# Performance work log

Measured on AMD Instinct MI355X. Metric: run time of the kernel, lower is better.

Reference implementation:

```python
import jax, jax.numpy as jnp
import numpy as np

NA, NM, H, RBF = 50000, 16384, 128, 64
GX, GY, GZ, B = 8, 8, 8, 32  # NM = B * GX*GY*GZ
E_AA, E_AM, E_MA = 800000, 400000, 400000
EPS = 1e-5


def setup_inputs() -> dict:
    key = jax.random.key(0)
    k = jax.random.split(key, 24)
    r = lambda i, s: jax.random.normal(k[i], s, jnp.float32)
    u = lambda i, s: jax.random.uniform(k[i], s, jnp.float32)
    ri = lambda i, s, hi: jax.random.randint(k[i], s, 0, hi, jnp.int32)
    return {
        "a_x": r(0, (NA, H)),
        "m_x": r(1, (NM, H)),
        "a2a_edge_index": ri(2, (2, E_AA), NA),
        "a2m_src": ri(3, (E_AM,), NA), "a2m_dst": ri(4, (E_AM,), NM),
        "m2a_src": ri(5, (E_MA,), NM), "m2a_dst": ri(6, (E_MA,), NA),
        "a2a_edge_weights": u(7, (E_AA,)),
        "a2m_edge_weights": u(8, (E_AM,)),
        "m2a_edge_weights": u(9, (E_MA,)),
        "a2a_edge_attr": r(10, (E_AA, RBF)),
        "a2m_edge_attr": r(11, (E_AM, RBF)),
        "m2a_edge_attr": r(12, (E_MA, RBF)),
        # message-passing params (node proj + RBF edge filter) per branch
        "W_short": r(13, (H, H)) / np.sqrt(H), "We_short": r(14, (RBF, H)) / np.sqrt(RBF),
        "W_a2m": r(15, (H, H)) / np.sqrt(H),  "We_a2m": r(16, (RBF, H)) / np.sqrt(RBF),
        "W_m2a": r(17, (H, H)) / np.sqrt(H),  "We_m2a": r(18, (RBF, H)) / np.sqrt(RBF),
        # long-range Conv3d (kernel 3, SAME padding)
        "conv_k": r(19, (H, H, 3, 3, 3)) / np.sqrt(H * 27), "conv_b": jnp.zeros((H,), jnp.float32),
        # LayerNorm affine params
        "g_short": jnp.ones((H,), jnp.float32), "b_short": jnp.zeros((H,), jnp.float32),
        "g_long": jnp.ones((H,), jnp.float32),  "b_long": jnp.zeros((H,), jnp.float32),
        "g_a2m": jnp.ones((H,), jnp.float32),   "b_a2m": jnp.zeros((H,), jnp.float32),
        "g_m2a": jnp.ones((H,), jnp.float32),   "b_m2a": jnp.zeros((H,), jnp.float32),
    }


def _ln(x, g, b):
    mu = x.mean(-1, keepdims=True)
    var = ((x - mu) ** 2).mean(-1, keepdims=True)
    return (x - mu) * jax.lax.rsqrt(var + EPS) * g + b


def _mp(x, src, dst, ew, ea, W, We, dim_size):
    # continuous-filter message pass: msg_e = (W x_src) * (We rbf_e) * w_e ; scatter-sum
    msg = (x[src] @ W) * (ea @ We) * ew[:, None]  # [E, H]
    return jax.ops.segment_sum(msg, dst, num_segments=dim_size)


def reference(a_x, m_x, a2a_edge_index, a2m_src, a2m_dst, m2a_src, m2a_dst,
              a2a_edge_weights, a2m_edge_weights, m2a_edge_weights,
              a2a_edge_attr, a2m_edge_attr, m2a_edge_attr,
              W_short, We_short, W_a2m, We_a2m, W_m2a, We_m2a,
              conv_k, conv_b,
              g_short, b_short, g_long, b_long, g_a2m, b_a2m, g_m2a, b_m2a):
    delta_a, delta_m = a_x, m_x
    # short-range atom branch
    a = _ln(a_x, g_short, b_short)
    a = _mp(a, a2a_edge_index[0], a2a_edge_index[1], a2a_edge_weights,
            a2a_edge_attr, W_short, We_short, NA)
    # long-range mesh branch: LN -> grid Conv3d (NCDHW) -> flatten back
    m = _ln(m_x, g_long, b_long)
    grid = m.reshape(B, GX, GY, GZ, H).transpose(0, 4, 1, 2, 3)  # [B,H,gx,gy,gz]
    grid = jax.lax.conv_general_dilated(
        grid, conv_k, window_strides=(1, 1, 1), padding='SAME',
        dimension_numbers=('NCDHW', 'OIDHW', 'NCDHW')) + conv_b[None, :, None, None, None]
    m = grid.transpose(0, 2, 3, 4, 1).reshape(-1, H)
    # cross messages with post-LN
    a2m_msg = _ln(_mp(a, a2m_src, a2m_dst, a2m_edge_weights, a2m_edge_attr,
                      W_a2m, We_a2m, NM), g_a2m, b_a2m)
    m2a_msg = _ln(_mp(m, m2a_src, m2a_dst, m2a_edge_weights, m2a_edge_attr,
                      W_m2a, We_m2a, NA), g_m2a, b_m2a)
    return (a + m2a_msg + delta_a, m + a2m_msg + delta_m)
```

## Files before the change

### kernel.cpp

```cpp
#include <hip/hip_runtime.h>
#include <hip/hip_bf16.h>

#define H 128
#define RBF 64

typedef __attribute__((ext_vector_type(8))) short bf16x8;
typedef __attribute__((ext_vector_type(4))) float f32x4;

__device__ inline short f2bf(float f) {
  union { float f; unsigned u; } v; v.f = f;
  const unsigned r = (v.u + 0x7FFFu + ((v.u >> 16) & 1u)) >> 16;
  return (short)r;
}

__global__ __launch_bounds__(128) void ln_rows(const float* __restrict__ X,
                                               const float* __restrict__ g,
                                               const float* __restrict__ bb,
                                               float* __restrict__ Y, int N) {
  __shared__ float sh[4];
  const int row = blockIdx.x;
  const int j = threadIdx.x;
  float x = X[(size_t)row * H + j];
  float s = x, q = x * x;
#pragma unroll
  for (int m = 32; m; m >>= 1) {
    s += __shfl_xor(s, m, 64);
    q += __shfl_xor(q, m, 64);
  }
  if ((j & 63) == 0) { sh[(j >> 6) * 2] = s; sh[(j >> 6) * 2 + 1] = q; }
  __syncthreads();
  s = sh[0] + sh[2];
  q = sh[1] + sh[3];
  const float mu = s * 0.0078125f;
  const float var = q * 0.0078125f - mu * mu;
  const float rs = rsqrtf(var + 1e-5f);
  Y[(size_t)row * H + j] = (x - mu) * rs * g[j] + bb[j];
}

__global__ __launch_bounds__(256) void pack_kt(const float* __restrict__ K,
                                               short* __restrict__ Ktb) {
  const int id = blockIdx.x * 256 + threadIdx.x;
  if (id >= 27 * 4 * 8 * 64) return;
  const int l = id & 63;
  int r = id >> 6;
  const int cb = r & 7; r >>= 3;
  const int kb = r & 3;
  const int tap = r >> 2;
  const int o = cb * 16 + (l & 15);
  const int i0 = kb * 32 + (l >> 4) * 8;
  short* out = Ktb + (size_t)id * 8;
#pragma unroll
  for (int j = 0; j < 8; ++j)
    out[j] = f2bf(K[((size_t)o * H + i0 + j) * 27 + tap]);
}

__global__ __launch_bounds__(256) void pack_we3(
    const float* __restrict__ We0, const float* __restrict__ We1,
    const float* __restrict__ We2, short* __restrict__ Wb0,
    short* __restrict__ Wb1, short* __restrict__ Wb2) {
  const int id = blockIdx.x * 256 + threadIdx.x;
  if (id >= 3072) return;
  const int which = id >> 10;
  const int i = id & 1023;
  const float* We = which == 0 ? We0 : which == 1 ? We1 : We2;
  short* Web = which == 0 ? Wb0 : which == 1 ? Wb1 : Wb2;
  const int f = i >> 6, l = i & 63;
  const int h = f >> 3, c = f & 7;
  const int col = (c << 4) + (l & 15);
  const int k0 = h * 32 + (l >> 4) * 8;
  short* o = Web + (size_t)i * 8;
#pragma unroll
  for (int j = 0; j < 8; ++j) o[j] = f2bf(We[(k0 + j) * H + col]);
}

__global__ __launch_bounds__(256) void k_hist3(
    const int* __restrict__ d0, const int* __restrict__ d1,
    const int* __restrict__ d2, int E0, int E1, int E2,
    int* __restrict__ cnt, int off1, int off2) {
  int i = blockIdx.x * 256 + threadIdx.x;
  const int stride = gridDim.x * 256;
  const int ET = E0 + E1 + E2;
  for (; i < ET; i += stride) {
    int d, off;
    if (i < E0) { d = d0[i]; off = 0; }
    else if (i < E0 + E1) { d = d1[i - E0]; off = off1; }
    else { d = d2[i - E0 - E1]; off = off2; }
    atomicAdd(&cnt[off + d], 1);
  }
}

__global__ __launch_bounds__(256) void k_blocksum(const int* __restrict__ cnt,
                                                  int* __restrict__ bsum) {
  __shared__ int sh[256];
  const int t = threadIdx.x;
  sh[t] = cnt[blockIdx.x * 256 + t];
  __syncthreads();
#pragma unroll
  for (int o = 128; o; o >>= 1) {
    if (t < o) sh[t] += sh[t + o];
    __syncthreads();
  }
  if (!t) bsum[blockIdx.x] = sh[0];
}

__global__ __launch_bounds__(512) void k_scan512(const int* __restrict__ bsum,
                                                 int* __restrict__ bpre, int NB) {
  __shared__ int sh[512];
  const int t = threadIdx.x;
  const int v = (t < NB) ? bsum[t] : 0;
  sh[t] = v;
  __syncthreads();
  for (int o = 1; o < 512; o <<= 1) {
    const int u = (t >= o) ? sh[t - o] : 0;
    __syncthreads();
    sh[t] += u;
    __syncthreads();
  }
  if (t < NB) bpre[t] = sh[t] - v;
}

__global__ __launch_bounds__(256) void k_apply3(
    const int* __restrict__ cnt, const int* __restrict__ bpre,
    int* __restrict__ rp0, int* __restrict__ rp1, int* __restrict__ rp2,
    int* __restrict__ cursor, int N0, int N1, int N2, int S1, int S2) {
  __shared__ int sh[256];
  const int b = blockIdx.x;
  const int t = threadIdx.x;
  const int gi = b * 256 + t;
  const int v = cnt[gi];
  sh[t] = v;
  __syncthreads();
  for (int o = 1; o < 256; o <<= 1) {
    const int u = (t >= o) ? sh[t - o] : 0;
    __syncthreads();
    sh[t] += u;
    __syncthreads();
  }
  int sb, N;
  int* rp;
  if (b < S1) { sb = 0; N = N0; rp = rp0; }
  else if (b < S2) { sb = S1; N = N1; rp = rp1; }
  else { sb = S2; N = N2; rp = rp2; }
  const int excl = sh[t] - v + bpre[b] - bpre[sb];
  const int il = (b - sb) * 256 + t;
  if (il <= N) {
    rp[il] = excl;
    if (il < N) cursor[gi] = excl;
  }
}

__global__ __launch_bounds__(256) void k_perm2w(
    const int* __restrict__ dst, const int* __restrict__ src,
    const float* __restrict__ ew, const float* __restrict__ ea, int E,
    int* __restrict__ cursor, int2* __restrict__ sd,
    short* __restrict__ eapfp) {
  const int lane = threadIdx.x & 63;
  const int wid = blockIdx.x * 4 + (threadIdx.x >> 6);
  const int nw = gridDim.x * 4;
  if (blockIdx.x == 0 && threadIdx.x < 16)
    sd[E + threadIdx.x] = make_int2(0, -1);
  const int r = lane >> 2;
  const int c = lane & 3;
  for (int ebase = wid * 16; ebase < E; ebase += nw * 16) {
    const int ecnt = min(16, E - ebase);
    int p = 0;
    float w = 0.f;
    if (lane < ecnt) {
      const int e = ebase + lane;
      const int d = dst[e];
      w = ew[e];
      p = atomicAdd(&cursor[d], 1);
      sd[p] = make_int2(src[e], d);
    }
    const int pr = __shfl(p, r, 64);
    const float wr = __shfl(w, r, 64);
    if (r < ecnt) {
      const float* er = ea + ((size_t)(ebase + r)) * RBF + c * 16;
      const float4 x0 = *(const float4*)(er);
      const float4 x1 = *(const float4*)(er + 4);
      const float4 x2 = *(const float4*)(er + 8);
      const float4 x3 = *(const float4*)(er + 12);
      bf16x8 o0, o1;
      o0[0] = f2bf(x0.x * wr); o0[1] = f2bf(x0.y * wr);
      o0[2] = f2bf(x0.z * wr); o0[3] = f2bf(x0.w * wr);
      o0[4] = f2bf(x1.x * wr); o0[5] = f2bf(x1.y * wr);
      o0[6] = f2bf(x1.z * wr); o0[7] = f2bf(x1.w * wr);
      o1[0] = f2bf(x2.x * wr); o1[1] = f2bf(x2.y * wr);
      o1[2] = f2bf(x2.z * wr); o1[3] = f2bf(x2.w * wr);
      o1[4] = f2bf(x3.x * wr); o1[5] = f2bf(x3.y * wr);
      o1[6] = f2bf(x3.z * wr); o1[7] = f2bf(x3.w * wr);
      short* ob = eapfp + (size_t)pr * RBF + c * 16;
      *(bf16x8*)(ob) = o0;
      *(bf16x8*)(ob + 8) = o1;
    }
  }
}

template <bool DO_LN>
__global__ __launch_bounds__(256) void proj_kernel(const float* __restrict__ X,
                                                   const float* __restrict__ W,
                                                   const float* __restrict__ g,
                                                   const float* __restrict__ bb,
                                                   float* __restrict__ Y, int N) {
  __shared__ float At[128 * 68];
  const int row0 = blockIdx.x * 64;
  const int t = threadIdx.x;
  const int lk = (t & 31) * 4;
  const int lr = t >> 5;
  float4 g4 = {0, 0, 0, 0}, b4 = {0, 0, 0, 0};
  if (DO_LN) {
    g4 = *(const float4*)(g + lk);
    b4 = *(const float4*)(bb + lk);
  }
#pragma unroll
  for (int p = 0; p < 8; ++p) {
    const int r = lr + p * 8;
    const int row = row0 + r;
    float4 xv = make_float4(0.f, 0.f, 0.f, 0.f);
    if (row < N) xv = *(const float4*)(X + (size_t)row * H + lk);
    if (DO_LN) {
      float s = xv.x + xv.y + xv.z + xv.w;
      float q = xv.x * xv.x + xv.y * xv.y + xv.z * xv.z + xv.w * xv.w;
#pragma unroll
      for (int m = 16; m; m >>= 1) {
        s += __shfl_xor(s, m, 64);
        q += __shfl_xor(q, m, 64);
      }
      const float mu = s * 0.0078125f;
      const float var = q * 0.0078125f - mu * mu;
      const float rs = rsqrtf(var + 1e-5f);
      xv.x = (xv.x - mu) * rs * g4.x + b4.x;
      xv.y = (xv.y - mu) * rs * g4.y + b4.y;
      xv.z = (xv.z - mu) * rs * g4.z + b4.z;
      xv.w = (xv.w - mu) * rs * g4.w + b4.w;
    }
    At[(lk + 0) * 68 + r] = xv.x;
    At[(lk + 1) * 68 + r] = xv.y;
    At[(lk + 2) * 68 + r] = xv.z;
    At[(lk + 3) * 68 + r] = xv.w;
  }
  __syncthreads();
  const int tc = t & 15;
  const int tr = t >> 4;
  float acc[4][8];
#pragma unroll
  for (int i = 0; i < 4; ++i)
#pragma unroll
    for (int c = 0; c < 8; ++c) acc[i][c] = 0.f;
  const float* wbase = W + tc * 8;
#pragma unroll 4
  for (int k = 0; k < 128; ++k) {
    const float4 a4 = *(const float4*)(At + k * 68 + tr * 4);
    const float4 w0 = *(const float4*)(wbase + k * H);
    const float4 w1 = *(const float4*)(wbase + k * H + 4);
    const float av[4] = {a4.x, a4.y, a4.z, a4.w};
#pragma unroll
    for (int i = 0; i < 4; ++i) {
      acc[i][0] += av[i] * w0.x; acc[i][1] += av[i] * w0.y;
      acc[i][2] += av[i] * w0.z; acc[i][3] += av[i] * w0.w;
      acc[i][4] += av[i] * w1.x; acc[i][5] += av[i] * w1.y;
      acc[i][6] += av[i] * w1.z; acc[i][7] += av[i] * w1.w;
    }
  }
#pragma unroll
  for (int i = 0; i < 4; ++i) {
    const int row = row0 + tr * 4 + i;
    if (row < N) {
      float4 o0 = {acc[i][0], acc[i][1], acc[i][2], acc[i][3]};
      float4 o1 = {acc[i][4], acc[i][5], acc[i][6], acc[i][7]};
      float* yp = Y + (size_t)row * H + tc * 8;
      *(float4*)yp = o0;
      *(float4*)(yp + 4) = o1;
    }
  }
}

template <int NPB, bool FUSE_LN>
__global__ __launch_bounds__(256, 3) void gather_mfma(
    const float* __restrict__ P, const short* __restrict__ Web,
    const short* __restrict__ eapfp, const int2* __restrict__ sd,
    const int* __restrict__ rowptr, int N, const float* __restrict__ base,
    const float* __restrict__ skip, const float* __restrict__ g,
    const float* __restrict__ bb, float* __restrict__ out) {
  constexpr int RSTR = (NPB + 1) * 132;
  constexpr int RPAD = RSTR + ((16 - (RSTR & 31)) & 31);
  __shared__ float acc[4 * RPAD];
  const int t = threadIdx.x;
  const int w = t >> 6, lane = t & 63;
  const int n0 = blockIdx.x * NPB;
  for (int u = t; u < 4 * RPAD; u += 256) acc[u] = 0.f;
  const int rp0 = rowptr[n0];
  const int rp1 = rowptr[min(n0 + NPB, N)];
  __syncthreads();
  const int q0 = rp0 >> 4;
  const int q1 = (rp1 + 15) >> 4;

  const int c0 = 2 * w;
  const bf16x8 bw0 = *(const bf16x8*)(Web + ((size_t)((0 + c0) * 64 + lane)) * 8);
  const bf16x8 bw1 = *(const bf16x8*)(Web + ((size_t)((8 + c0) * 64 + lane)) * 8);
  const bf16x8 bw2 = *(const bf16x8*)(Web + ((size_t)((1 + c0) * 64 + lane)) * 8);
  const bf16x8 bw3 = *(const bf16x8*)(Web + ((size_t)((9 + c0) * 64 + lane)) * 8);

  const int l15 = lane & 15, lg = lane >> 4, rbase = lg * 4;
  const int col0 = c0 * 16 + l15;
  float* const arep = acc + lg * RPAD;

  auto LOADI = [&](int q, bf16x8& A0, bf16x8& A1, int4& sp, int4& dp) {
    const short* fb = eapfp + ((size_t)(q * 16 + l15)) * RBF + lg * 8;
    A0 = *(const bf16x8*)(fb);
    A1 = *(const bf16x8*)(fb + 32);
    const int4 sd01 = *(const int4*)(sd + (size_t)(q * 16 + rbase));
    const int4 sd23 = *(const int4*)(sd + (size_t)(q * 16 + rbase + 2));
    sp = make_int4(sd01.x, sd01.z, sd23.x, sd23.z);
    dp = make_int4(sd01.y, sd01.w, sd23.y, sd23.w);
  };
  auto PLOAD = [&](const int4& sp, float* pv) {
    const float* p0 = P + (size_t)sp.x * H + col0;
    const float* p1 = P + (size_t)sp.y * H + col0;
    const float* p2 = P + (size_t)sp.z * H + col0;
    const float* p3 = P + (size_t)sp.w * H + col0;
    pv[0] = p0[0]; pv[4] = p0[16];
    pv[1] = p1[0]; pv[5] = p1[16];
    pv[2] = p2[0]; pv[6] = p2[16];
    pv[3] = p3[0]; pv[7] = p3[16];
  };
  auto COMP = [&](const bf16x8& A0, const bf16x8& A1, const float* pv,
                  const int4& dp) {
    f32x4 C0 = {0.f, 0.f, 0.f, 0.f};
    C0 = __builtin_amdgcn_mfma_f32_16x16x32_bf16(A0, bw0, C0, 0, 0, 0);
    C0 = __builtin_amdgcn_mfma_f32_16x16x32_bf16(A1, bw1, C0, 0, 0, 0);
    f32x4 C1 = {0.f, 0.f, 0.f, 0.f};
    C1 = __builtin_amdgcn_mfma_f32_16x16x32_bf16(A0, bw2, C1, 0, 0, 0);
    C1 = __builtin_amdgcn_mfma_f32_16x16x32_bf16(A1, bw3, C1, 0, 0, 0);
    const int dls[4] = {dp.x - n0, dp.y - n0, dp.z - n0, dp.w - n0};
    int dl[5];
#pragma unroll
    for (int j = 0; j < 4; ++j)
      dl[j] = ((unsigned)dls[j] < (unsigned)NPB) ? dls[j] : NPB;
    dl[4] = -1;
    float c0v = 0.f, c1v = 0.f;
#pragma unroll
    for (int j = 0; j < 4; ++j) {
      c0v += C0[j] * pv[j];
      c1v += C1[j] * pv[4 + j];
      if (dl[j + 1] != dl[j]) {
        float* a0 = arep + dl[j] * 132 + col0;
        a0[0] += c0v;
        a0[16] += c1v;
        c0v = 0.f;
        c1v = 0.f;
      }
    }
  };

  if (q1 > q0) {
    bf16x8 A0a, A1a, A0b, A1b;
    int4 spa, dpa, spb, dpb;
    float pva[8], pvb[8];
    LOADI(q0, A0a, A1a, spa, dpa);
    PLOAD(spa, pva);
    for (int q = q0; q < q1; q += 2) {
      if (q + 1 < q1) { LOADI(q + 1, A0b, A1b, spb, dpb); PLOAD(spb, pvb); }
      COMP(A0a, A1a, pva, dpa);
      if (q + 2 < q1) { LOADI(q + 2, A0a, A1a, spa, dpa); PLOAD(spa, pva); }
      if (q + 1 < q1) COMP(A0b, A1b, pvb, dpb);
    }
  }
  __syncthreads();

  for (int n = w; n < NPB; n += 4) {
    const int node = n0 + n;
    if (node >= N) break;
    const int rb = n * 132 + lane;
    const float v0 = acc[rb] + acc[RPAD + rb] + acc[2 * RPAD + rb] +
                     acc[3 * RPAD + rb];
    const float v1 = acc[rb + 64] + acc[RPAD + rb + 64] +
                     acc[2 * RPAD + rb + 64] + acc[3 * RPAD + rb + 64];
    const size_t i0 = (size_t)node * H + lane;
    if (FUSE_LN) {
      float s = v0 + v1, q = v0 * v0 + v1 * v1;
#pragma unroll
      for (int m = 32; m; m >>= 1) {
        s += __shfl_xor(s, m, 64);
        q += __shfl_xor(q, m, 64);
      }
      const float mu = s * 0.0078125f;
      const float var = q * 0.0078125f - mu * mu;
      const float rs = rsqrtf(var + 1e-5f);
      out[i0] = base[i0] + (v0 - mu) * rs * g[lane] + bb[lane] + skip[i0];
      out[i0 + 64] =
          base[i0 + 64] + (v1 - mu) * rs * g[lane + 64] + bb[lane + 64] + skip[i0 + 64];
    } else {
      out[i0] = v0;
      out[i0 + 64] = v1;
    }
  }
}

__global__ __launch_bounds__(256, 2) void conv3d_mfma(
    const float* __restrict__ Min, const short* __restrict__ Ktb,
    const float* __restrict__ bias, float* __restrict__ Mout) {
  __shared__ short in_s[193 * 128];
  const int b = blockIdx.x >> 3;
  const int x = blockIdx.x & 7;
  const int t = threadIdx.x;
  const int w = t >> 6, lane = t & 63;
  const int l15 = lane & 15, lg = lane >> 4;

  if (t < 128) in_s[192 * 128 + t] = 0;
#pragma unroll
  for (int it = 0; it < 12; ++it) {
    const int gidx = it * 256 + t;
    const int r = gidx >> 4;
    const int ch = (gidx & 15) * 8;
    const int gx = x + (r >> 6) - 1;
    const int yz = r & 63;
    float4 v0 = make_float4(0.f, 0.f, 0.f, 0.f), v1 = v0;
    if (gx >= 0 && gx < 8) {
      const float* src = Min + ((size_t)((b * 8 + gx) * 64 + yz)) * H + ch;
      v0 = *(const float4*)(src);
      v1 = *(const float4*)(src + 4);
    }
    bf16x8 pk;
    pk[0] = f2bf(v0.x); pk[1] = f2bf(v0.y); pk[2] = f2bf(v0.z); pk[3] = f2bf(v0.w);
    pk[4] = f2bf(v1.x); pk[5] = f2bf(v1.y); pk[6] = f2bf(v1.z); pk[7] = f2bf(v1.w);
    const int byte0 = (r * 256 + ch * 2) ^ ((r & 7) << 4);
    *(bf16x8*)((char*)in_s + byte0) = pk;
  }
  __syncthreads();

  const int cb0 = 2 * w;
  f32x4 C[4][2];
#pragma unroll
  for (int mt = 0; mt < 4; ++mt) {
    C[mt][0] = (f32x4){0.f, 0.f, 0.f, 0.f};
    C[mt][1] = (f32x4){0.f, 0.f, 0.f, 0.f};
  }

  auto BP = [&](int u, int cbi) -> const bf16x8* {
    return (const bf16x8*)(Ktb + (((size_t)u * 8) + cb0 + cbi) * 64 * 8 +
                           (size_t)lane * 8);
  };
  bf16x8 Ba0 = *BP(0, 0), Ba1 = *BP(0, 1);
  for (int u = 0; u < 108; ++u) {
    const int un = min(u + 1, 107);
    const bf16x8 Bn0 = *BP(un, 0);
    const bf16x8 Bn1 = *BP(un, 1);
    const int tap = u >> 2, kb = u & 3;
    const int dx = tap / 9, dy = (tap / 3) % 3, dz = tap % 3;
#pragma unroll
    for (int mt = 0; mt < 4; ++mt) {
      const int v = mt * 16 + l15;
      const int y = v >> 3, z = v & 7;
      const int ny = y + dy - 1, nz = z + dz - 1;
      const bool ok = (ny >= 0 && ny < 8 && nz >= 0 && nz < 8);
      const int vrow = ok ? dx * 64 + ny * 8 + nz : 192;
      const int byte0 = ((vrow * 256 + kb * 64 + lg * 16) ^ ((vrow & 7) << 4));
      const bf16x8 A = *(const bf16x8*)((const char*)in_s + byte0);
      C[mt][0] = __builtin_amdgcn_mfma_f32_16x16x32_bf16(A, Ba0, C[mt][0], 0, 0, 0);
      C[mt][1] = __builtin_amdgcn_mfma_f32_16x16x32_bf16(A, Ba1, C[mt][1], 0, 0, 0);
    }
    Ba0 = Bn0;
    Ba1 = Bn1;
  }

  const float b0 = bias[cb0 * 16 + l15];
  const float b1 = bias[cb0 * 16 + 16 + l15];
  float* obase = Mout + ((size_t)((b * 8 + x) * 64)) * H;
#pragma unroll
  for (int mt = 0; mt < 4; ++mt)
#pragma unroll
    for (int j = 0; j < 4; ++j) {
      const int vox = mt * 16 + lg * 4 + j;
      float* op = obase + (size_t)vox * H + cb0 * 16 + l15;
      op[0] = C[mt][0][j] + b0;
      op[16] = C[mt][1][j] + b1;
    }
}

extern "C" void kernel_launch(void* const* d_in, const int* in_sizes, int n_in,
                              void* d_out, int out_size, void* d_ws, size_t ws_size,
                              hipStream_t stream) {
  const float* a_x = (const float*)d_in[0];
  const float* m_x = (const float*)d_in[1];
  const int* aa_idx = (const int*)d_in[2];
  const int* a2m_src = (const int*)d_in[3];
  const int* a2m_dst = (const int*)d_in[4];
  const int* m2a_src = (const int*)d_in[5];
  const int* m2a_dst = (const int*)d_in[6];
  const float* aa_w = (const float*)d_in[7];
  const float* a2m_w = (const float*)d_in[8];
  const float* m2a_w = (const float*)d_in[9];
  const float* aa_ea = (const float*)d_in[10];
  const float* a2m_ea = (const float*)d_in[11];
  const float* m2a_ea = (const float*)d_in[12];
  const float* W_short = (const float*)d_in[13];
  const float* We_short = (const float*)d_in[14];
  const float* W_a2m = (const float*)d_in[15];
  const float* We_a2m = (const float*)d_in[16];
  const float* W_m2a = (const float*)d_in[17];
  const float* We_m2a = (const float*)d_in[18];
  const float* conv_k = (const float*)d_in[19];
  const float* conv_b = (const float*)d_in[20];
  const float* g_short = (const float*)d_in[21];
  const float* b_short = (const float*)d_in[22];
  const float* g_long = (const float*)d_in[23];
  const float* b_long = (const float*)d_in[24];
  const float* g_a2m = (const float*)d_in[25];
  const float* b_a2m = (const float*)d_in[26];
  const float* g_m2a = (const float*)d_in[27];
  const float* b_m2a = (const float*)d_in[28];

  const int NA = in_sizes[0] / H;
  const int NM = in_sizes[1] / H;
  const int E_AA = in_sizes[2] / 2;
  const int E_AM = in_sizes[3];
  const int E_MA = in_sizes[5];
  const int* aa_src = aa_idx;
  const int* aa_dst = aa_idx + E_AA;

  const int NB_A = (NA + 256) / 256;
  const int NB_M = (NM + 256) / 256;
  const int S1 = NB_A, S2 = NB_A + NB_M;
  const int NB_T = NB_A + NB_M + NB_A;
  const int OFF1 = S1 * 256, OFF2 = S2 * 256;

  float* ws = (float*)d_ws;
  float* p_buf = ws;
  float* m1_buf = p_buf + (size_t)NA * H;
  float* m2_buf = m1_buf + (size_t)NM * H;
  float* a2_buf = m2_buf + (size_t)NM * H;
  short* web_aa = (short*)(a2_buf + (size_t)NA * H);
  short* web_a2m = web_aa + 8192;
  short* web_m2a = web_a2m + 8192;
  short* ktb = web_m2a + 8192;
  short* eapfp = ktb + 442368;
  int2* sd_aa = (int2*)(eapfp + (size_t)E_AA * RBF);
  int2* sd_a2m = sd_aa + E_AA + 16;
  int2* sd_m2a = sd_a2m + E_AM + 16;
  int* iws = (int*)(sd_m2a + E_MA + 16);
  int* cnt = iws;       iws += NB_T * 256;
  int* cursor = iws;    iws += NB_T * 256;
  int* bsum = iws;      iws += 512;
  int* bpre = iws;      iws += 512;
  int* rp_aa = iws;     iws += NA + 1;
  int* rp_a2m = iws;    iws += NM + 1;
  int* rp_m2a = iws;    iws += NA + 1;

  float* out_a = (float*)d_out;
  float* out_m = out_a + (size_t)NA * H;

  pack_we3<<<12, 256, 0, stream>>>(We_short, We_a2m, We_m2a, web_aa, web_a2m,
                                   web_m2a);
  pack_kt<<<(27 * 4 * 8 * 64 + 255) / 256, 256, 0, stream>>>(conv_k, ktb);
  ln_rows<<<NM, 128, 0, stream>>>(m_x, g_long, b_long, m1_buf, NM);
  conv3d_mfma<<<(NM / 64), 256, 0, stream>>>(m1_buf, ktb, conv_b, m2_buf);
  proj_kernel<true><<<(NA + 63) / 64, 256, 0, stream>>>(a_x, W_short, g_short,
                                                        b_short, p_buf, NA);

  hipMemsetAsync(cnt, 0, (size_t)NB_T * 256 * sizeof(int), stream);
  k_hist3<<<2048, 256, 0, stream>>>(aa_dst, a2m_dst, m2a_dst, E_AA, E_AM, E_MA,
                                    cnt, OFF1, OFF2);
  k_blocksum<<<NB_T, 256, 0, stream>>>(cnt, bsum);
  k_scan512<<<1, 512, 0, stream>>>(bsum, bpre, NB_T);
  k_apply3<<<NB_T, 256, 0, stream>>>(cnt, bpre, rp_aa, rp_a2m, rp_m2a, cursor,
                                     NA, NM, NA, S1, S2);

  k_perm2w<<<2048, 256, 0, stream>>>(aa_dst, aa_src, aa_w, aa_ea, E_AA, cursor,
                                     sd_aa, eapfp);
  gather_mfma<16, false><<<(NA + 15) / 16, 256, 0, stream>>>(
      p_buf, web_aa, eapfp, sd_aa, rp_aa, NA, nullptr, nullptr, nullptr,
      nullptr, a2_buf);

  proj_kernel<false><<<(NA + 63) / 64, 256, 0, stream>>>(a2_buf, W_a2m, nullptr,
                                                         nullptr, p_buf, NA);
  k_perm2w<<<2048, 256, 0, stream>>>(a2m_dst, a2m_src, a2m_w, a2m_ea, E_AM,
                                     cursor + OFF1, sd_a2m, eapfp);
  gather_mfma<16, true><<<(NM + 15) / 16, 256, 0, stream>>>(
      p_buf, web_a2m, eapfp, sd_a2m, rp_a2m, NM, m2_buf, m_x, g_a2m, b_a2m,
      out_m);

  proj_kernel<false><<<(NM + 63) / 64, 256, 0, stream>>>(m2_buf, W_m2a, nullptr,
                                                         nullptr, m1_buf, NM);
  k_perm2w<<<2048, 256, 0, stream>>>(m2a_dst, m2a_src, m2a_w, m2a_ea, E_MA,
                                     cursor + OFF2, sd_m2a, eapfp);
  gather_mfma<16, true><<<(NA + 15) / 16, 256, 0, stream>>>(
      m1_buf, web_m2a, eapfp, sd_m2a, rp_m2a, NA, a2_buf, a_x, g_m2a, b_m2a,
      out_a);
}
```

Before: 623.3 us.

## Move node projections to bf16 MFMA and deepen gather prefetch pipeline

Replaces the FP32 FMA projection kernel with an MFMA-based kernel. It stages activations as bf16 in swizzled shared memory and reads pre-packed bf16 weights produced by a new packing kernel. The LayerNorm that was fused into the first projection is split out into a separate ln_rows pass, which adds an extra buffer write and read. The gather kernel's software pipeline goes from two-stage to three-stage prefetch, merging index and P loads to hide more gather latency at the cost of registers. Converting X to bf16 for the projections lowers precision.

Result: faster. 557.7 us (-10.5%).

```diff
diff --git a/kernel.cpp b/kernel.cpp
--- a/kernel.cpp
+++ b/kernel.cpp
@@ -71,6 +71,25 @@
   short* o = Web + (size_t)i * 8;
 #pragma unroll
   for (int j = 0; j < 8; ++j) o[j] = f2bf(We[(k0 + j) * H + col]);
+}
+
+__global__ __launch_bounds__(256) void pack_w3(
+    const float* __restrict__ W0, const float* __restrict__ W1,
+    const float* __restrict__ W2, short* __restrict__ Wb0,
+    short* __restrict__ Wb1, short* __restrict__ Wb2) {
+  const int id = blockIdx.x * 256 + threadIdx.x;
+  if (id >= 3 * 2048) return;
+  const int which = id >> 11;
+  const int i = id & 2047;
+  const float* W = which == 0 ? W0 : which == 1 ? W1 : W2;
+  short* Wb = which == 0 ? Wb0 : which == 1 ? Wb1 : Wb2;
+  const int f = i >> 6, l = i & 63;
+  const int kb = f >> 3, cb = f & 7;
+  const int col = cb * 16 + (l & 15);
+  const int k0 = kb * 32 + (l >> 4) * 8;
+  short* o = Wb + (size_t)i * 8;
+#pragma unroll
+  for (int j = 0; j < 8; ++j) o[j] = f2bf(W[(size_t)(k0 + j) * H + col]);
 }
 
 __global__ __launch_bounds__(256) void k_hist3(
@@ -196,83 +215,72 @@
   }
 }
 
-template <bool DO_LN>
-__global__ __launch_bounds__(256) void proj_kernel(const float* __restrict__ X,
-                                                   const float* __restrict__ W,
-                                                   const float* __restrict__ g,
-                                                   const float* __restrict__ bb,
-                                                   float* __restrict__ Y, int N) {
-  __shared__ float At[128 * 68];
+__global__ __launch_bounds__(256, 2) void proj_mfma(
+    const float* __restrict__ X, const short* __restrict__ Wb,
+    float* __restrict__ Y, int N) {
+  __shared__ short xs[64 * 128];
   const int row0 = blockIdx.x * 64;
   const int t = threadIdx.x;
-  const int lk = (t & 31) * 4;
-  const int lr = t >> 5;
-  float4 g4 = {0, 0, 0, 0}, b4 = {0, 0, 0, 0};
-  if (DO_LN) {
-    g4 = *(const float4*)(g + lk);
-    b4 = *(const float4*)(bb + lk);
-  }
-#pragma unroll
-  for (int p = 0; p < 8; ++p) {
-    const int r = lr + p * 8;
+  const int w = t >> 6, lane = t & 63;
+  const int l15 = lane & 15, lg = lane >> 4;
+
+#pragma unroll
+  for (int it = 0; it < 4; ++it) {
+    const int gidx = it * 256 + t;
+    const int r = gidx >> 4;
+    const int ch = (gidx & 15) * 8;
     const int row = row0 + r;
-    float4 xv = make_float4(0.f, 0.f, 0.f, 0.f);
-    if (row < N) xv = *(const float4*)(X + (size_t)row * H + lk);
-    if (DO_LN) {
-      float s = xv.x + xv.y + xv.z + xv.w;
-      float q = xv.x * xv.x + xv.y * xv.y + xv.z * xv.z + xv.w * xv.w;
-#pragma unroll
-      for (int m = 16; m; m >>= 1) {
-        s += __shfl_xor(s, m, 64);
-        q += __shfl_xor(q, m, 64);
+    float4 v0 = make_float4(0.f, 0.f, 0.f, 0.f), v1 = v0;
+    if (row < N) {
+      const float* src = X + (size_t)row * H + ch;
+      v0 = *(const float4*)(src);
+      v1 = *(const float4*)(src + 4);
+    }
+    bf16x8 pk;
+    pk[0] = f2bf(v0.x); pk[1] = f2bf(v0.y); pk[2] = f2bf(v0.z); pk[3] = f2bf(v0.w);
+    pk[4] = f2bf(v1.x); pk[5] = f2bf(v1.y); pk[6] = f2bf(v1.z); pk[7] = f2bf(v1.w);
+    const int byte0 = (r * 256 + ch * 2) ^ ((r & 7) << 4);
+    *(bf16x8*)((char*)xs + byte0) = pk;
+  }
+  __syncthreads();
+
+  const int cb0 = 2 * w;
+  bf16x8 bw[4][2];
+#pragma unroll
+  for (int kb = 0; kb < 4; ++kb)
+#pragma unroll
+    for (int ci = 0; ci < 2; ++ci)
+      bw[kb][ci] = *(const bf16x8*)(Wb + (((size_t)kb * 8 + cb0 + ci) * 64 +
+                                          lane) * 8);
+
+  f32x4 C[4][2];
+#pragma unroll
+  for (int mt = 0; mt < 4; ++mt) {
+    C[mt][0] = (f32x4){0.f, 0.f, 0.f, 0.f};
+    C[mt][1] = (f32x4){0.f, 0.f, 0.f, 0.f};
+  }
+#pragma unroll
+  for (int kb = 0; kb < 4; ++kb) {
+#pragma unroll
+    for (int mt = 0; mt < 4; ++mt) {
+      const int r = mt * 16 + l15;
+      const int byte0 = (r * 256 + kb * 64 + lg * 16) ^ ((r & 7) << 4);
+      const bf16x8 A = *(const bf16x8*)((const char*)xs + byte0);
+      C[mt][0] = __builtin_amdgcn_mfma_f32_16x16x32_bf16(A, bw[kb][0], C[mt][0], 0, 0, 0);
+      C[mt][1] = __builtin_amdgcn_mfma_f32_16x16x32_bf16(A, bw[kb][1], C[mt][1], 0, 0, 0);
+    }
+  }
+#pragma unroll
+  for (int mt = 0; mt < 4; ++mt)
+#pragma unroll
+    for (int j = 0; j < 4; ++j) {
+      const int row = row0 + mt * 16 + lg * 4 + j;
+      if (row < N) {
+        float* yp = Y + (size_t)row * H + cb0 * 16 + l15;
+        yp[0] = C[mt][0][j];
+        yp[16] = C[mt][1][j];
       }
-      const float mu = s * 0.0078125f;
-      const float var = q * 0.0078125f - mu * mu;
-      const float rs = rsqrtf(var + 1e-5f);
-      xv.x = (xv.x - mu) * rs * g4.x + b4.x;
-      xv.y = (xv.y - mu) * rs * g4.y + b4.y;
-      xv.z = (xv.z - mu) * rs * g4.z + b4.z;
-      xv.w = (xv.w - mu) * rs * g4.w + b4.w;
-    }
-    At[(lk + 0) * 68 + r] = xv.x;
-    At[(lk + 1) * 68 + r] = xv.y;
-    At[(lk + 2) * 68 + r] = xv.z;
-    At[(lk + 3) * 68 + r] = xv.w;
-  }
-  __syncthreads();
-  const int tc = t & 15;
-  const int tr = t >> 4;
-  float acc[4][8];
-#pragma unroll
-  for (int i = 0; i < 4; ++i)
-#pragma unroll
-    for (int c = 0; c < 8; ++c) acc[i][c] = 0.f;
-  const float* wbase = W + tc * 8;
-#pragma unroll 4
-  for (int k = 0; k < 128; ++k) {
-    const float4 a4 = *(const float4*)(At + k * 68 + tr * 4);
-    const float4 w0 = *(const float4*)(wbase + k * H);
-    const float4 w1 = *(const float4*)(wbase + k * H + 4);
-    const float av[4] = {a4.x, a4.y, a4.z, a4.w};
-#pragma unroll
-    for (int i = 0; i < 4; ++i) {
-      acc[i][0] += av[i] * w0.x; acc[i][1] += av[i] * w0.y;
-      acc[i][2] += av[i] * w0.z; acc[i][3] += av[i] * w0.w;
-      acc[i][4] += av[i] * w1.x; acc[i][5] += av[i] * w1.y;
-      acc[i][6] += av[i] * w1.z; acc[i][7] += av[i] * w1.w;
-    }
-  }
-#pragma unroll
-  for (int i = 0; i < 4; ++i) {
-    const int row = row0 + tr * 4 + i;
-    if (row < N) {
-      float4 o0 = {acc[i][0], acc[i][1], acc[i][2], acc[i][3]};
-      float4 o1 = {acc[i][4], acc[i][5], acc[i][6], acc[i][7]};
-      float* yp = Y + (size_t)row * H + tc * 8;
-      *(float4*)yp = o0;
-      *(float4*)(yp + 4) = o1;
-    }
-  }
+    }
 }
 
 template <int NPB, bool FUSE_LN>
@@ -305,7 +313,8 @@
   const int col0 = c0 * 16 + l15;
   float* const arep = acc + lg * RPAD;
 
-  auto LOADI = [&](int q, bf16x8& A0, bf16x8& A1, int4& sp, int4& dp) {
+  auto LOAD = [&](int q, bf16x8& A0, bf16x8& A1, int4& sp, int4& dp,
+                  float* pv) {
     const short* fb = eapfp + ((size_t)(q * 16 + l15)) * RBF + lg * 8;
     A0 = *(const bf16x8*)(fb);
     A1 = *(const bf16x8*)(fb + 32);
@@ -313,8 +322,6 @@
     const int4 sd23 = *(const int4*)(sd + (size_t)(q * 16 + rbase + 2));
     sp = make_int4(sd01.x, sd01.z, sd23.x, sd23.z);
     dp = make_int4(sd01.y, sd01.w, sd23.y, sd23.w);
-  };
-  auto PLOAD = [&](const int4& sp, float* pv) {
     const float* p0 = P + (size_t)sp.x * H + col0;
     const float* p1 = P + (size_t)sp.y * H + col0;
     const float* p2 = P + (size_t)sp.z * H + col0;
@@ -354,16 +361,22 @@
   };
 
   if (q1 > q0) {
-    bf16x8 A0a, A1a, A0b, A1b;
-    int4 spa, dpa, spb, dpb;
-    float pva[8], pvb[8];
-    LOADI(q0, A0a, A1a, spa, dpa);
-    PLOAD(spa, pva);
-    for (int q = q0; q < q1; q += 2) {
-      if (q + 1 < q1) { LOADI(q + 1, A0b, A1b, spb, dpb); PLOAD(spb, pvb); }
+    bf16x8 A0a, A1a, A0b, A1b, A0c, A1c;
+    int4 spa, dpa, spb, dpb, spc, dpc;
+    float pva[8], pvb[8], pvc[8];
+    LOAD(q0, A0a, A1a, spa, dpa, pva);
+    if (q0 + 1 < q1) LOAD(q0 + 1, A0b, A1b, spb, dpb, pvb);
+    int q = q0;
+    while (true) {
+      if (q + 2 < q1) LOAD(q + 2, A0c, A1c, spc, dpc, pvc);
       COMP(A0a, A1a, pva, dpa);
-      if (q + 2 < q1) { LOADI(q + 2, A0a, A1a, spa, dpa); PLOAD(spa, pva); }
-      if (q + 1 < q1) COMP(A0b, A1b, pvb, dpb);
+      if (++q >= q1) break;
+      if (q + 2 < q1) LOAD(q + 2, A0a, A1a, spa, dpa, pva);
+      COMP(A0b, A1b, pvb, dpb);
+      if (++q >= q1) break;
+      if (q + 2 < q1) LOAD(q + 2, A0b, A1b, spb, dpb, pvb);
+      COMP(A0c, A1c, pvc, dpc);
+      if (++q >= q1) break;
     }
   }
   __syncthreads();
@@ -530,10 +543,14 @@
   float* m1_buf = p_buf + (size_t)NA * H;
   float* m2_buf = m1_buf + (size_t)NM * H;
   float* a2_buf = m2_buf + (size_t)NM * H;
-  short* web_aa = (short*)(a2_buf + (size_t)NA * H);
+  float* a1_buf = a2_buf + (size_t)NA * H;
+  short* web_aa = (short*)(a1_buf + (size_t)NA * H);
   short* web_a2m = web_aa + 8192;
   short* web_m2a = web_a2m + 8192;
-  short* ktb = web_m2a + 8192;
+  short* wb_s = web_m2a + 8192;
+  short* wb_a2m = wb_s + 16384;
+  short* wb_m2a = wb_a2m + 16384;
+  short* ktb = wb_m2a + 16384;
   short* eapfp = ktb + 442368;
   int2* sd_aa = (int2*)(eapfp + (size_t)E_AA * RBF);
   int2* sd_a2m = sd_aa + E_AA + 16;
@@ -552,11 +569,12 @@
 
   pack_we3<<<12, 256, 0, stream>>>(We_short, We_a2m, We_m2a, web_aa, web_a2m,
                                    web_m2a);
+  pack_w3<<<24, 256, 0, stream>>>(W_short, W_a2m, W_m2a, wb_s, wb_a2m, wb_m2a);
   pack_kt<<<(27 * 4 * 8 * 64 + 255) / 256, 256, 0, stream>>>(conv_k, ktb);
   ln_rows<<<NM, 128, 0, stream>>>(m_x, g_long, b_long, m1_buf, NM);
   conv3d_mfma<<<(NM / 64), 256, 0, stream>>>(m1_buf, ktb, conv_b, m2_buf);
-  proj_kernel<true><<<(NA + 63) / 64, 256, 0, stream>>>(a_x, W_short, g_short,
-                                                        b_short, p_buf, NA);
+  ln_rows<<<NA, 128, 0, stream>>>(a_x, g_short, b_short, a1_buf, NA);
+  proj_mfma<<<(NA + 63) / 64, 256, 0, stream>>>(a1_buf, wb_s, p_buf, NA);
 
   hipMemsetAsync(cnt, 0, (size_t)NB_T * 256 * sizeof(int), stream);
   k_hist3<<<2048, 256, 0, stream>>>(aa_dst, a2m_dst, m2a_dst, E_AA, E_AM, E_MA,
@@ -572,16 +590,14 @@
       p_buf, web_aa, eapfp, sd_aa, rp_aa, NA, nullptr, nullptr, nullptr,
       nullptr, a2_buf);
 
-  proj_kernel<false><<<(NA + 63) / 64, 256, 0, stream>>>(a2_buf, W_a2m, nullptr,
-                                                         nullptr, p_buf, NA);
+  proj_mfma<<<(NA + 63) / 64, 256, 0, stream>>>(a2_buf, wb_a2m, p_buf, NA);
   k_perm2w<<<2048, 256, 0, stream>>>(a2m_dst, a2m_src, a2m_w, a2m_ea, E_AM,
                                      cursor + OFF1, sd_a2m, eapfp);
   gather_mfma<16, true><<<(NM + 15) / 16, 256, 0, stream>>>(
       p_buf, web_a2m, eapfp, sd_a2m, rp_a2m, NM, m2_buf, m_x, g_a2m, b_a2m,
       out_m);
 
-  proj_kernel<false><<<(NM + 63) / 64, 256, 0, stream>>>(m2_buf, W_m2a, nullptr,
-                                                         nullptr, m1_buf, NM);
+  proj_mfma<<<(NM + 63) / 64, 256, 0, stream>>>(m2_buf, wb_m2a, m1_buf, NM);
   k_perm2w<<<2048, 256, 0, stream>>>(m2a_dst, m2a_src, m2a_w, m2a_ea, E_MA,
                                      cursor + OFF2, sd_m2a, eapfp);
   gather_mfma<16, true><<<(NA + 15) / 16, 256, 0, stream>>>(
```
